# Performance work log

Hardware: AMD Instinct MI355X
Metric: run time of the kernel (lower is better)

## Reference

```python
import jax, jax.numpy as jnp
import numpy as np
from jax import lax

B = 512
P_KEEP = 0.5  # base dropout keep probability (p=0.5)


def conv(x, w, b, pad):
    y = lax.conv_general_dilated(x, w, (1, 1), [(pad, pad), (pad, pad)],
                                 dimension_numbers=('NCHW', 'OIHW', 'NCHW'))
    return y + b[None, :, None, None]


def maxpool3s2(x):
    return lax.reduce_window(x, -jnp.inf, lax.max, (1, 1, 3, 3), (1, 1, 2, 2), 'VALID')


def eb_linear(p_out, a, W):
    # Excitation backprop through a linear layer (bias ignored).
    # p_out: [B, out] marginal winning probs at layer output
    # a:     [B, in]  (non-negative) activations at layer input
    # W:     [out, in]
    Wp = jnp.maximum(W, 0.0)
    z = a @ Wp.T                              # [B, out]
    s = jnp.where(z > 0, p_out / z, 0.0)      # [B, out]
    return a * (s @ Wp)                       # [B, in]


def setup_inputs() -> dict:
    key = jax.random.key(0)
    ks = jax.random.split(key, 16)

    def w(k, shape, fan_in):
        return (jax.random.normal(k, shape, jnp.float32) / np.sqrt(fan_in)).astype(jnp.float32)

    return {
        'x': jax.random.normal(ks[0], (B, 3, 32, 32), jnp.float32),
        'noise': jax.random.uniform(ks[1], (B, 2048), jnp.float32),
        'conv1_w': w(ks[2], (96, 3, 5, 5), 3 * 25),
        'conv1_b': jnp.zeros((96,), jnp.float32),
        'conv2_w': w(ks[3], (128, 96, 5, 5), 96 * 25),
        'conv2_b': jnp.zeros((128,), jnp.float32),
        'conv3_w': w(ks[4], (256, 128, 5, 5), 128 * 25),
        'conv3_b': jnp.zeros((256,), jnp.float32),
        'fc1_w': w(ks[5], (2048, 1024), 1024),
        'fc1_b': jnp.zeros((2048,), jnp.float32),
        'fc2_w': w(ks[6], (2048, 2048), 2048),
        'fc2_b': jnp.zeros((2048,), jnp.float32),
        'fc3_w': w(ks[7], (10, 2048), 2048),
        'fc3_b': jnp.zeros((10,), jnp.float32),
        'label': jax.random.randint(ks[8], (B,), 0, 10),
    }


def reference(x, noise, conv1_w, conv1_b, conv2_w, conv2_b, conv3_w, conv3_b,
              fc1_w, fc1_b, fc2_w, fc2_b, fc3_w, fc3_b, label):
    h1 = maxpool3s2(jax.nn.relu(conv(x, conv1_w, conv1_b, 1)))   # [B,96,14,14]
    h2 = maxpool3s2(jax.nn.relu(conv(h1, conv2_w, conv2_b, 2)))  # [B,128,6,6]
    h3 = maxpool3s2(jax.nn.relu(conv(h2, conv3_w, conv3_b, 2)))  # [B,256,2,2]
    h4 = h3.reshape(h3.shape[0], -1)                             # [B,1024]
    h5 = jax.nn.relu(h4 @ fc1_w.T + fc1_b)                       # [B,2048]

    # --- Excitation backprop through latterModel (fc2 -> relu -> fc3), batched ---
    h6_eb = jax.nn.relu(h5 @ fc2_w.T + fc2_b)                    # [B,2048]
    p_out = jax.nn.one_hot(label, 10, dtype=h5.dtype)            # [B,10]
    p_h6 = eb_linear(p_out, h6_eb, fc3_w)                        # [B,2048]
    pebs = eb_linear(p_h6, h5, fc2_w)                            # [B,2048]

    # --- Excitation Dropout mask ---
    N = pebs.shape[1]
    num = (1.0 - P_KEEP) * (N - 1) * pebs
    retain_p = 1.0 - num / (num + P_KEEP * (1.0 - pebs))         # [B,2048]
    mask = (noise < retain_p).astype(h5.dtype)
    h_ed = jnp.where(retain_p > 0, h5 * mask / retain_p, 0.0)

    h6 = jax.nn.relu(h_ed @ fc2_w.T + fc2_b)                     # [B,2048]
    return h6 @ fc3_w.T + fc3_b                                  # [B,10]
```

## Files before the change

kernel.cpp:

```cpp
#include <hip/hip_runtime.h>
#include <hip/hip_bf16.h>


typedef __attribute__((ext_vector_type(8))) short bf16x8;
typedef __attribute__((ext_vector_type(4))) float f32x4;

__device__ __forceinline__ void split_bf16(float x, ushort& h, ushort& l) {
    __hip_bfloat16 bh = __float2bfloat16(x);
    float fh = __bfloat162float(bh);
    __hip_bfloat16 bl = __float2bfloat16(x - fh);
    h = *(ushort*)&bh;
    l = *(ushort*)&bl;
}

__device__ __forceinline__ void split3_bf16(float x, ushort& a, ushort& b,
                                            ushort& c) {
    __hip_bfloat16 ba = __float2bfloat16(x);
    float fa = __bfloat162float(ba);
    float r = x - fa;
    __hip_bfloat16 bb = __float2bfloat16(r);
    float fb = __bfloat162float(bb);
    __hip_bfloat16 bc = __float2bfloat16(r - fb);
    a = *(ushort*)&ba;
    b = *(ushort*)&bb;
    c = *(ushort*)&bc;
}

__device__ __forceinline__ void gld_lds16(const void* g, void* l) {
    __builtin_amdgcn_global_load_lds(
        (const __attribute__((address_space(1))) unsigned int*)g,
        (__attribute__((address_space(3))) unsigned int*)l, 16, 0, 0);
}

__global__ void zero_k(float4* __restrict__ p, int n4) {
    int idx = blockIdx.x * 256 + threadIdx.x;
    int stride = gridDim.x * 256;
    float4 z = {0.f, 0.f, 0.f, 0.f};
    for (int i = idx; i < n4; i += stride) p[i] = z;
}

__global__ void transw_k(const float* __restrict__ in, float* __restrict__ out,
                         int OC, int K) {
    int idx = blockIdx.x * 256 + threadIdx.x;
    if (idx >= OC * K) return;
    int oc = idx / K, k = idx % K;
    out[k * OC + oc] = in[idx];
}

__global__ void splitw_k(const float* __restrict__ in, ushort* __restrict__ hi,
                         ushort* __restrict__ lo, int OC, int IC) {
    int idx = blockIdx.x * 256 + threadIdx.x;
    if (idx >= OC * IC * 25) return;
    int oc = idx / (IC * 25);
    int r = idx % (IC * 25);
    int ic = r / 25, tap = r % 25;
    float v = in[idx];
    ushort h, l;
    split_bf16(v, h, l);
    size_t k = (size_t)oc * IC * 25 + tap * IC + ic;
    hi[k] = h;
    lo[k] = l;
}

__global__ void splitw3_k(const float* __restrict__ in, ushort* __restrict__ out,
                          int off, int total) {
    int idx = blockIdx.x * 256 + threadIdx.x;
    if (idx >= total) return;
    ushort a, b, c;
    split3_bf16(in[idx], a, b, c);
    out[idx] = a;
    out[idx + off] = b;
    out[idx + 2 * off] = c;
}

__global__ __launch_bounds__(256) void splitw3t_relu_k(
        const float* __restrict__ in, ushort* __restrict__ out, int off) {
    __shared__ float tile[64][65];
    const int bx = blockIdx.x & 31, by = blockIdx.x >> 5;
    const int j = threadIdx.x & 63, i0 = threadIdx.x >> 6;
    for (int i = i0; i < 64; i += 4)
        tile[i][j] = in[(size_t)(by * 64 + i) * 2048 + bx * 64 + j];
    __syncthreads();
    for (int r = i0; r < 64; r += 4) {
        float x = fmaxf(tile[j][r], 0.f);
        ushort a, b, c;
        split3_bf16(x, a, b, c);
        size_t o = (size_t)(bx * 64 + r) * 2048 + by * 64 + j;
        out[o] = a;
        out[o + off] = b;
        out[o + 2 * off] = c;
    }
}

__global__ __launch_bounds__(256) void conv1_v3(
        const float* __restrict__ x, const float* __restrict__ w1t,
        const float* __restrict__ b1, ushort* __restrict__ h1hi,
        ushort* __restrict__ h1lo) {
    __shared__ float simg[3 * 34 * 34];
    __shared__ float c1s[8][904];
    const int b = blockIdx.x, oc0 = blockIdx.y * 8, t = threadIdx.x;

    for (int i = t; i < 3 * 34 * 34; i += 256) simg[i] = 0.f;
    __syncthreads();
    for (int i = t; i < 3072; i += 256) {
        int ic = i >> 10, r = (i >> 5) & 31, c = i & 31;
        simg[ic * 1156 + (r + 1) * 34 + (c + 1)] = x[(size_t)b * 3072 + i];
    }
    __syncthreads();

    int base[4];
    bool valid[4];
#pragma unroll
    for (int j = 0; j < 4; j++) {
        int p = t + j * 256;
        valid[j] = p < 900;
        int oh = p / 30, ow = p % 30;
        base[j] = valid[j] ? oh * 34 + ow : 0;
    }

    float acc[4][8];
#pragma unroll
    for (int j = 0; j < 4; j++)
#pragma unroll
        for (int u = 0; u < 8; u++) acc[j][u] = 0.f;

#pragma unroll 1
    for (int ic = 0; ic < 3; ic++) {
        const int icb = ic * 1156;
#pragma unroll 1
        for (int kh = 0; kh < 5; kh++) {
#pragma unroll
            for (int kw = 0; kw < 5; kw++) {
                const float4* wr =
                    (const float4*)&w1t[(ic * 25 + kh * 5 + kw) * 96 + oc0];
                float4 w0 = wr[0], w1v = wr[1];
#pragma unroll
                for (int j = 0; j < 4; j++) {
                    float v = simg[icb + base[j] + kh * 34 + kw];
#pragma unroll
                    for (int u = 0; u < 4; u++) {
                        acc[j][u] = fmaf((&w0.x)[u], v, acc[j][u]);
                        acc[j][u + 4] = fmaf((&w1v.x)[u], v, acc[j][u + 4]);
                    }
                }
            }
        }
    }
#pragma unroll
    for (int j = 0; j < 4; j++)
        if (valid[j]) {
            int p = t + j * 256;
#pragma unroll
            for (int u = 0; u < 8; u++) c1s[u][p] = acc[j][u];
        }
    __syncthreads();
    if (t < 196) {
        const int ph = t / 14, pw = t % 14;
        ushort hv[8], lv[8];
#pragma unroll
        for (int u = 0; u < 8; u++) {
            float m = c1s[u][(2 * ph) * 30 + 2 * pw];
#pragma unroll
            for (int q = 1; q < 9; q++) {
                int dy = q / 3, dx = q % 3;
                m = fmaxf(m, c1s[u][(2 * ph + dy) * 30 + 2 * pw + dx]);
            }
            float o = fmaxf(m + b1[oc0 + u], 0.f);
            split_bf16(o, hv[u], lv[u]);
        }
        size_t ob = (((size_t)b * 18 + ph + 2) * 18 + pw + 2) * 96 + oc0;
        *(bf16x8*)&h1hi[ob] = *(bf16x8*)&hv[0];
        *(bf16x8*)&h1lo[ob] = *(bf16x8*)&lv[0];
    }
}

template <int BM, int IC, int H, int W, int OH, int OW, int OC, int NM>
__global__ __launch_bounds__(256, 2) void convmfma5_k(
        const ushort* __restrict__ ah, int aoff,
        const ushort* __restrict__ wh, int boff,
        const float* __restrict__ bias, float* __restrict__ C) {
    constexpr int K = 25 * IC;
    constexpr int MI = BM / 32;
    constexpr int G = NM * (OC / 128);
    __shared__ ushort At[2][BM * 64];
    __shared__ ushort Bt[2][128 * 64];
    const int t = threadIdx.x;
    const int lane = t & 63, wv = t >> 6;
    const int id = blockIdx.x;
    const int id2 = (id & 7) * (G >> 3) + (id >> 3);
    const int n0 = (id2 / NM) * 128;
    const int m0 = (id2 % NM) * BM;
    const int wm = (wv >> 1) * (BM / 2);
    const int wn = (wv & 1) * 64;

    const int srow = lane >> 3;
    const int slot = lane & 7;
    const int part = slot ^ srow;
    const bool hiA = part < 4;
    const int pk = (part & 3) * 8;

    int arb[MI];
#pragma unroll
    for (int rr = 0; rr < MI; rr++) {
        int r = wv * (BM / 4) + rr * 8 + srow;
        int m = m0 + r;
        int b = m / (OH * OW), pxy = m % (OH * OW);
        int oh = pxy / OW, ow = pxy % OW;
        arb[rr] = ((b * H + oh) * W + ow) * IC + pk;
    }
    const ushort* __restrict__ aptr = ah + (hiA ? 0 : aoff);
    size_t brb[4];
#pragma unroll
    for (int rr = 0; rr < 4; rr++) {
        int r = wv * 32 + rr * 8 + srow;
        brb[rr] = (size_t)(n0 + r) * K + pk;
    }
    const ushort* __restrict__ bptr = wh + (hiA ? 0 : boff);

    f32x4 acc[MI][4];
#pragma unroll
    for (int i = 0; i < MI; i++)
#pragma unroll
        for (int j = 0; j < 4; j++) acc[i][j] = (f32x4)(0.f);

    const int q = lane >> 4;
    const int fr = lane & 15;

    auto stage = [&](int buf, int k0s) {
        const int tap = k0s / IC;
        const int koff = ((tap / 5) * W + (tap % 5)) * IC + (k0s - tap * IC);
#pragma unroll
        for (int rr = 0; rr < MI; rr++)
            gld_lds16(aptr + arb[rr] + koff,
                      &At[buf][(wv * (BM / 4) + rr * 8) * 64]);
#pragma unroll
        for (int rr = 0; rr < 4; rr++)
            gld_lds16(bptr + brb[rr] + k0s,
                      &Bt[buf][(wv * 32 + rr * 8) * 64]);
    };

    stage(0, 0);
    __syncthreads();

    int cur = 0;
#pragma unroll 1
    for (int k0 = 0; k0 < K; k0 += 32) {
        bf16x8 afh[MI], afl[MI], bfh[4], bfl[4];
#pragma unroll
        for (int i = 0; i < MI; i++) {
            int row = wm + fr + i * 16;
            afh[i] = *(const bf16x8*)&At[cur][row * 64 + ((q ^ (row & 7)) << 3)];
            afl[i] = *(const bf16x8*)&At[cur][row * 64 + (((4 | q) ^ (row & 7)) << 3)];
        }
#pragma unroll
        for (int j = 0; j < 4; j++) {
            int row = wn + fr + j * 16;
            bfh[j] = *(const bf16x8*)&Bt[cur][row * 64 + ((q ^ (row & 7)) << 3)];
            bfl[j] = *(const bf16x8*)&Bt[cur][row * 64 + (((4 | q) ^ (row & 7)) << 3)];
        }
        const int nxt = k0 + 32;
        if (nxt < K) stage(cur ^ 1, nxt);

#pragma unroll
        for (int i = 0; i < MI; i++)
#pragma unroll
            for (int j = 0; j < 4; j++) {
                acc[i][j] = __builtin_amdgcn_mfma_f32_16x16x32_bf16(
                    afh[i], bfh[j], acc[i][j], 0, 0, 0);
                acc[i][j] = __builtin_amdgcn_mfma_f32_16x16x32_bf16(
                    afh[i], bfl[j], acc[i][j], 0, 0, 0);
                acc[i][j] = __builtin_amdgcn_mfma_f32_16x16x32_bf16(
                    afl[i], bfh[j], acc[i][j], 0, 0, 0);
            }
        __syncthreads();
        cur ^= 1;
    }

    const int crow0 = (lane >> 4) * 4;
    const int ccol = lane & 15;
#pragma unroll
    for (int i = 0; i < MI; i++) {
        int gm = m0 + wm + i * 16 + crow0;
#pragma unroll
        for (int j = 0; j < 4; j++) {
            int gn = n0 + wn + j * 16 + ccol;
            float bb = bias[gn];
#pragma unroll
            for (int r = 0; r < 4; r++)
                C[(size_t)(gm + r) * OC + gn] = acc[i][j][r] + bb;
        }
    }
}

__global__ void pool2_k(const float* __restrict__ in, ushort* __restrict__ ohi,
                        ushort* __restrict__ olo) {
    int idx = blockIdx.x * 256 + threadIdx.x;
    if (idx >= 512 * 36 * 128) return;
    int c = idx & 127;
    int tmp = idx >> 7;
    int pw = tmp % 6;
    int tmp2 = tmp / 6;
    int ph = tmp2 % 6;
    int b = tmp2 / 6;
    size_t base = (((size_t)b * 14 + 2 * ph) * 14 + 2 * pw) * 128 + c;
    float m = -3.4e38f;
#pragma unroll
    for (int dy = 0; dy < 3; dy++)
#pragma unroll
        for (int dx = 0; dx < 3; dx++)
            m = fmaxf(m, in[base + (dy * 14 + dx) * 128]);
    float v = fmaxf(m, 0.f);
    ushort h, l;
    split_bf16(v, h, l);
    size_t o = (((size_t)b * 10 + ph + 2) * 10 + pw + 2) * 128 + c;
    ohi[o] = h;
    olo[o] = l;
}

__global__ void pool3_k(const float* __restrict__ in, float* __restrict__ h3) {
    int idx = blockIdx.x * 256 + threadIdx.x;
    if (idx >= 512 * 4 * 256) return;
    int c = idx & 255;
    int pw = (idx >> 8) & 1;
    int ph = (idx >> 9) & 1;
    int b = idx >> 10;
    size_t base = (((size_t)b * 6 + 2 * ph) * 6 + 2 * pw) * 256 + c;
    float m = -3.4e38f;
#pragma unroll
    for (int dy = 0; dy < 3; dy++)
#pragma unroll
        for (int dx = 0; dx < 3; dx++)
            m = fmaxf(m, in[base + (dy * 6 + dx) * 256]);
    h3[(size_t)b * 1024 + c * 4 + ph * 2 + pw] = fmaxf(m, 0.f);
}

template <int TRANSB, int RELUW, int BIAS, int RELUOUT, int DUAL>
__global__ __launch_bounds__(256, 2) void gemm2_k(
        const float* __restrict__ A, const float* __restrict__ Bm,
        const float* __restrict__ bias, float* __restrict__ C,
        float* __restrict__ C2, int K, int N) {
    __shared__ float As[16][36];
    __shared__ float Bs[16][68];
    __shared__ float Bs2[DUAL ? 16 : 1][68];
    const int t = threadIdx.x;
    const int n0 = blockIdx.x * 64;
    const int m0 = blockIdx.y * 32;
    const int tm = t >> 5, tn = t & 31;

    float acc[8];
    float acc2[DUAL ? 8 : 1];
#pragma unroll
    for (int i = 0; i < 8; i++) acc[i] = 0.f;
    if constexpr (DUAL) {
#pragma unroll
        for (int i = 0; i < 8; i++) acc2[i] = 0.f;
    }

    const int r4 = t >> 2, k4 = (t & 3) << 2;

    for (int k0 = 0; k0 < K; k0 += 16) {
        float4 av;
        if (t < 128) av = *(const float4*)&A[(size_t)(m0 + r4) * K + k0 + k4];
        float4 bv;
        if constexpr (TRANSB) {
            bv = *(const float4*)&Bm[(size_t)(n0 + r4) * K + k0 + k4];
        } else {
            bv = *(const float4*)&Bm[(size_t)(k0 + (t >> 4)) * N + n0 + ((t & 15) << 2)];
        }
        if constexpr (RELUW) {
            bv.x = fmaxf(bv.x, 0.f); bv.y = fmaxf(bv.y, 0.f);
            bv.z = fmaxf(bv.z, 0.f); bv.w = fmaxf(bv.w, 0.f);
        }
        __syncthreads();
        if (t < 128) {
            As[k4 + 0][r4] = av.x; As[k4 + 1][r4] = av.y;
            As[k4 + 2][r4] = av.z; As[k4 + 3][r4] = av.w;
        }
        if constexpr (TRANSB) {
            Bs[k4 + 0][r4] = bv.x; Bs[k4 + 1][r4] = bv.y;
            Bs[k4 + 2][r4] = bv.z; Bs[k4 + 3][r4] = bv.w;
            if constexpr (DUAL) {
                Bs2[k4 + 0][r4] = fmaxf(bv.x, 0.f);
                Bs2[k4 + 1][r4] = fmaxf(bv.y, 0.f);
                Bs2[k4 + 2][r4] = fmaxf(bv.z, 0.f);
                Bs2[k4 + 3][r4] = fmaxf(bv.w, 0.f);
            }
        } else {
            *(float4*)&Bs[t >> 4][(t & 15) << 2] = bv;
        }
        __syncthreads();
#pragma unroll
        for (int kk = 0; kk < 16; kk++) {
            float4 a4 = *(const float4*)&As[kk][tm * 4];
            float2 b2 = *(const float2*)&Bs[kk][tn * 2];
            const float* ap = &a4.x;
            const float* bp = &b2.x;
            if constexpr (DUAL) {
                float2 b2p = *(const float2*)&Bs2[kk][tn * 2];
                const float* bpp = &b2p.x;
#pragma unroll
                for (int i = 0; i < 4; i++)
#pragma unroll
                    for (int j = 0; j < 2; j++) {
                        acc[i * 2 + j] = fmaf(ap[i], bp[j], acc[i * 2 + j]);
                        acc2[i * 2 + j] = fmaf(ap[i], bpp[j], acc2[i * 2 + j]);
                    }
            } else {
#pragma unroll
                for (int i = 0; i < 4; i++)
#pragma unroll
                    for (int j = 0; j < 2; j++)
                        acc[i * 2 + j] = fmaf(ap[i], bp[j], acc[i * 2 + j]);
            }
        }
    }

#pragma unroll
    for (int i = 0; i < 4; i++) {
        size_t row = (size_t)(m0 + tm * 4 + i) * N + n0 + tn * 2;
        float2 o;
#pragma unroll
        for (int j = 0; j < 2; j++) {
            float v = acc[i * 2 + j];
            if constexpr (BIAS) v += bias[n0 + tn * 2 + j];
            if constexpr (RELUOUT) v = fmaxf(v, 0.f);
            (&o.x)[j] = v;
        }
        *(float2*)&C[row] = o;
        if constexpr (DUAL) {
            float2 o2;
#pragma unroll
            for (int j = 0; j < 2; j++) (&o2.x)[j] = acc2[i * 2 + j];
            *(float2*)&C2[row] = o2;
        }
    }
}

template <int BIAS, int RELUOUT, int DUAL>
__global__ __launch_bounds__(256, 2) void gemmfc_k(
        const float* __restrict__ A, const ushort* __restrict__ B3, int boff,
        const float* __restrict__ bias, float* __restrict__ C,
        float* __restrict__ C2, int K, int N) {
    __shared__ ushort Aa[32][40], Ab[32][40], Ac[32][40];
    __shared__ ushort Ba[64][40], Bb[64][40], Bc[64][40];
    const int t = threadIdx.x;
    const int n0 = blockIdx.x * 64;
    const int m0 = blockIdx.y * 32;
    const int lane = t & 63, wv = t >> 6;
    const int wm = (wv >> 1) * 16, wn = (wv & 1) * 32;
    const int fr = lane & 15, kp = (lane >> 4) * 8;

    f32x4 acc[2], acc2[DUAL ? 2 : 1];
#pragma unroll
    for (int j = 0; j < 2; j++) acc[j] = (f32x4)(0.f);
    if constexpr (DUAL) {
#pragma unroll
        for (int j = 0; j < 2; j++) acc2[j] = (f32x4)(0.f);
    }

    const int ar = t >> 2, ak = (t & 3) * 8;

    for (int k0 = 0; k0 < K; k0 += 32) {
        float4 a0, a1;
        if (t < 128) {
            a0 = *(const float4*)&A[(size_t)(m0 + ar) * K + k0 + ak];
            a1 = *(const float4*)&A[(size_t)(m0 + ar) * K + k0 + ak + 4];
        }
        size_t bidx = (size_t)(n0 + ar) * K + k0 + ak;
        bf16x8 b0 = *(const bf16x8*)&B3[bidx];
        bf16x8 b1 = *(const bf16x8*)&B3[bidx + boff];
        bf16x8 b2 = *(const bf16x8*)&B3[bidx + 2 * (size_t)boff];
        __syncthreads();
        if (t < 128) {
            ushort sa[8], sb[8], sc[8];
#pragma unroll
            for (int e = 0; e < 4; e++)
                split3_bf16((&a0.x)[e], sa[e], sb[e], sc[e]);
#pragma unroll
            for (int e = 0; e < 4; e++)
                split3_bf16((&a1.x)[e], sa[4 + e], sb[4 + e], sc[4 + e]);
            *(bf16x8*)&Aa[ar][ak] = *(bf16x8*)sa;
            *(bf16x8*)&Ab[ar][ak] = *(bf16x8*)sb;
            *(bf16x8*)&Ac[ar][ak] = *(bf16x8*)sc;
        }
        *(bf16x8*)&Ba[ar][ak] = b0;
        *(bf16x8*)&Bb[ar][ak] = b1;
        *(bf16x8*)&Bc[ar][ak] = b2;
        __syncthreads();

        bf16x8 fa = *(const bf16x8*)&Aa[wm + fr][kp];
        bf16x8 fb = *(const bf16x8*)&Ab[wm + fr][kp];
        bf16x8 fc = *(const bf16x8*)&Ac[wm + fr][kp];
#pragma unroll
        for (int j = 0; j < 2; j++) {
            int row = wn + j * 16 + fr;
            bf16x8 ga = *(const bf16x8*)&Ba[row][kp];
            bf16x8 gb = *(const bf16x8*)&Bb[row][kp];
            bf16x8 gc = *(const bf16x8*)&Bc[row][kp];
            acc[j] = __builtin_amdgcn_mfma_f32_16x16x32_bf16(fa, ga, acc[j], 0, 0, 0);
            acc[j] = __builtin_amdgcn_mfma_f32_16x16x32_bf16(fa, gb, acc[j], 0, 0, 0);
            acc[j] = __builtin_amdgcn_mfma_f32_16x16x32_bf16(fb, ga, acc[j], 0, 0, 0);
            acc[j] = __builtin_amdgcn_mfma_f32_16x16x32_bf16(fa, gc, acc[j], 0, 0, 0);
            acc[j] = __builtin_amdgcn_mfma_f32_16x16x32_bf16(fc, ga, acc[j], 0, 0, 0);
            acc[j] = __builtin_amdgcn_mfma_f32_16x16x32_bf16(fb, gb, acc[j], 0, 0, 0);
            if constexpr (DUAL) {
                bf16x8 msk = ga >> 15;
                bf16x8 ra = ga & ~msk;
                bf16x8 rb = gb & ~msk;
                bf16x8 rc = gc & ~msk;
                acc2[j] = __builtin_amdgcn_mfma_f32_16x16x32_bf16(fa, ra, acc2[j], 0, 0, 0);
                acc2[j] = __builtin_amdgcn_mfma_f32_16x16x32_bf16(fa, rb, acc2[j], 0, 0, 0);
                acc2[j] = __builtin_amdgcn_mfma_f32_16x16x32_bf16(fb, ra, acc2[j], 0, 0, 0);
                acc2[j] = __builtin_amdgcn_mfma_f32_16x16x32_bf16(fa, rc, acc2[j], 0, 0, 0);
                acc2[j] = __builtin_amdgcn_mfma_f32_16x16x32_bf16(fc, ra, acc2[j], 0, 0, 0);
                acc2[j] = __builtin_amdgcn_mfma_f32_16x16x32_bf16(fb, rb, acc2[j], 0, 0, 0);
            }
        }
    }

    const int gm0 = m0 + wm + (lane >> 4) * 4;
#pragma unroll
    for (int j = 0; j < 2; j++) {
        int gn = n0 + wn + j * 16 + fr;
        float bb = BIAS ? bias[gn] : 0.f;
#pragma unroll
        for (int r = 0; r < 4; r++) {
            float v = acc[j][r] + bb;
            if constexpr (RELUOUT) v = fmaxf(v, 0.f);
            C[(size_t)(gm0 + r) * N + gn] = v;
            if constexpr (DUAL) C2[(size_t)(gm0 + r) * N + gn] = acc2[j][r];
        }
    }
}

__global__ __launch_bounds__(256) void zlab_k(
        const float* __restrict__ h6eb, const float* __restrict__ w3,
        const int* __restrict__ label, float* __restrict__ zlab) {
    __shared__ float red[4];
    const int b = blockIdx.x, t = threadIdx.x;
    const int lab = label[b];
    const float4* hp = (const float4*)(h6eb + (size_t)b * 2048);
    const float4* wp = (const float4*)(w3 + (size_t)lab * 2048);
    float s = 0.f;
    for (int i = t; i < 512; i += 256) {
        float4 h = hp[i], w = wp[i];
        s += h.x * fmaxf(w.x, 0.f) + h.y * fmaxf(w.y, 0.f) +
             h.z * fmaxf(w.z, 0.f) + h.w * fmaxf(w.w, 0.f);
    }
#pragma unroll
    for (int off = 32; off > 0; off >>= 1) s += __shfl_down(s, off, 64);
    if ((t & 63) == 0) red[t >> 6] = s;
    __syncthreads();
    if (t == 0) zlab[b] = red[0] + red[1] + red[2] + red[3];
}

__global__ void s2_k(const float* __restrict__ h6eb, const float* __restrict__ z2,
                     const float* __restrict__ w3, const int* __restrict__ label,
                     const float* __restrict__ zlab, float* __restrict__ s2) {
    int idx = blockIdx.x * 256 + threadIdx.x;
    int b = idx >> 11, j = idx & 2047;
    float zl = zlab[b], zv = z2[idx];
    float v = 0.f;
    if (zl > 0.f && zv > 0.f) {
        float wp = fmaxf(w3[(size_t)label[b] * 2048 + j], 0.f);
        v = h6eb[idx] * wp / (zl * zv);
    }
    s2[idx] = v;
}

__global__ void edrop_k(const float* __restrict__ h5, const float* __restrict__ t,
                        const float* __restrict__ noise, float* __restrict__ hed) {
    int idx = blockIdx.x * 256 + threadIdx.x;
    float pe = h5[idx] * t[idx];
    float num = 1023.5f * pe;
    float retain = 1.f - num / (num + 0.5f * (1.f - pe));
    float m = (noise[idx] < retain) ? 1.f : 0.f;
    hed[idx] = (retain > 0.f) ? h5[idx] * m / retain : 0.f;
}

__global__ void fc3_out_k(const float* __restrict__ h6, const float* __restrict__ w,
                          const float* __restrict__ bias, float* __restrict__ out) {
    int idx = blockIdx.x * 256 + threadIdx.x;
    if (idx >= 5120) return;
    int b = idx / 10, c = idx % 10;
    const float4* hp = (const float4*)(h6 + (size_t)b * 2048);
    const float4* wp = (const float4*)(w + (size_t)c * 2048);
    float s = 0.f;
    for (int i = 0; i < 512; i++) {
        float4 h = hp[i], ww = wp[i];
        s += h.x * ww.x + h.y * ww.y + h.z * ww.z + h.w * ww.w;
    }
    out[idx] = s + bias[c];
}

extern "C" void kernel_launch(void* const* d_in, const int* in_sizes, int n_in,
                              void* d_out, int out_size, void* d_ws, size_t ws_size,
                              hipStream_t stream) {
    const float* x       = (const float*)d_in[0];
    const float* noise   = (const float*)d_in[1];
    const float* conv1_w = (const float*)d_in[2];
    const float* conv1_b = (const float*)d_in[3];
    const float* conv2_w = (const float*)d_in[4];
    const float* conv2_b = (const float*)d_in[5];
    const float* conv3_w = (const float*)d_in[6];
    const float* conv3_b = (const float*)d_in[7];
    const float* fc1_w   = (const float*)d_in[8];
    const float* fc1_b   = (const float*)d_in[9];
    const float* fc2_w   = (const float*)d_in[10];
    const float* fc2_b   = (const float*)d_in[11];
    const float* fc3_w   = (const float*)d_in[12];
    const float* fc3_b   = (const float*)d_in[13];
    const int*   label   = (const int*)d_in[14];
    float* out = (float*)d_out;

    const size_t N_H1 = (size_t)512 * 18 * 18 * 96;
    const size_t N_C2 = (size_t)512 * 14 * 14 * 128;
    const size_t N_H2 = (size_t)512 * 10 * 10 * 128;
    const size_t N_H3 = (size_t)512 * 1024;

    float* ws = (float*)d_ws;
    ushort* h1hi = (ushort*)ws;
    ushort* h1lo = h1hi + N_H1;
    float* c3 = ws;
    float* c2 = ws + N_H1;
    float* h5   = c2;
    float* h6eb = c2 + 1 * 1048576;
    float* z2   = c2 + 2 * 1048576;
    float* s2   = c2 + 3 * 1048576;
    float* tb   = c2 + 4 * 1048576;
    float* hed  = c2 + 5 * 1048576;
    float* h6   = c2 + 6 * 1048576;
    float* zlab = c2 + 7 * 1048576;
    ushort* h2hi = (ushort*)(ws + N_H1 + N_C2);
    ushort* h2lo = h2hi + N_H2;
    float* h3  = ws + N_H1 + N_C2 + N_H2;
    float* w1t = h3 + N_H3;
    ushort* w2sh = (ushort*)(w1t + 7200);
    ushort* w2sl = w2sh + 307200;
    ushort* w3sh = w2sl + 307200;
    ushort* w3sl = w3sh + 819200;
    ushort* w23  = w3sl + 819200;
    ushort* w2rt = w23 + 3 * 4194304;

    transw_k<<<(75 * 96 + 255) / 256, 256, 0, stream>>>(conv1_w, w1t, 96, 75);
    splitw_k<<<(307200 + 255) / 256, 256, 0, stream>>>(conv2_w, w2sh, w2sl, 128, 96);
    splitw_k<<<(819200 + 255) / 256, 256, 0, stream>>>(conv3_w, w3sh, w3sl, 256, 128);
    splitw3_k<<<16384, 256, 0, stream>>>(fc2_w, w23, 4194304, 4194304);
    splitw3t_relu_k<<<1024, 256, 0, stream>>>(fc2_w, w2rt, 4194304);

    zero_k<<<2048, 256, 0, stream>>>((float4*)h1hi, (int)(N_H1 / 4));
    zero_k<<<2048, 256, 0, stream>>>((float4*)h2hi, (int)(N_H2 / 4));

    conv1_v3<<<dim3(512, 12), 256, 0, stream>>>(x, w1t, conv1_b, h1hi, h1lo);
    convmfma5_k<128, 96, 18, 18, 14, 14, 128, 784><<<784, 256, 0, stream>>>(
        h1hi, (int)N_H1, w2sh, 307200, conv2_b, c2);
    pool2_k<<<(512 * 36 * 128 + 255) / 256, 256, 0, stream>>>(c2, h2hi, h2lo);
    convmfma5_k<64, 128, 10, 10, 6, 6, 256, 288><<<576, 256, 0, stream>>>(
        h2hi, (int)N_H2, w3sh, 819200, conv3_b, c3);
    pool3_k<<<(512 * 4 * 256 + 255) / 256, 256, 0, stream>>>(c3, h3);

    gemm2_k<1, 0, 1, 1, 0><<<dim3(32, 16), 256, 0, stream>>>(
        h3, fc1_w, fc1_b, h5, nullptr, 1024, 2048);

    gemmfc_k<1, 1, 1><<<dim3(32, 16), 256, 0, stream>>>(
        h5, w23, 4194304, fc2_b, h6eb, z2, 2048, 2048);

    zlab_k<<<512, 256, 0, stream>>>(h6eb, fc3_w, label, zlab);
    s2_k<<<4096, 256, 0, stream>>>(h6eb, z2, fc3_w, label, zlab, s2);

    gemmfc_k<0, 0, 0><<<dim3(32, 16), 256, 0, stream>>>(
        s2, w2rt, 4194304, nullptr, tb, nullptr, 2048, 2048);

    edrop_k<<<4096, 256, 0, stream>>>(h5, tb, noise, hed);

    gemmfc_k<1, 1, 0><<<dim3(32, 16), 256, 0, stream>>>(
        hed, w23, 4194304, fc2_b, h6, nullptr, 2048, 2048);

    fc3_out_k<<<20, 256, 0, stream>>>(h6, fc3_w, fc3_b, out);
}
```

Before: 839.0 us.

## Stage conv weights through registers and run fc1 on split-bf16 MFMA GEMM

The conv MFMA kernel now keeps a single LDS buffer for the weight tile. Weights are prefetched into registers one step ahead and written to LDS at the start of each iteration, and the kernel adds explicit waitcnt/barrier handling, setprio around the MFMA block, and a higher occupancy hint. Separately, fc1 moves from a scalar fp32 SIMT GEMM to the existing three-way bf16-split MFMA gemmfc kernel, which needs an extra weight-split pass. The changes aim to cut LDS pressure, raise occupancy, and speed up fc1, but they add register pressure and an extra preprocessing kernel.

New measurement: 855.3 us. No clear change (+1.9%).

```diff
diff --git a/kernel.cpp b/kernel.cpp
--- a/kernel.cpp
+++ b/kernel.cpp
@@ -175,7 +175,7 @@
 }
 
 template <int BM, int IC, int H, int W, int OH, int OW, int OC, int NM>
-__global__ __launch_bounds__(256, 2) void convmfma5_k(
+__global__ __launch_bounds__(256, 3) void convmfma6_k(
         const ushort* __restrict__ ah, int aoff,
         const ushort* __restrict__ wh, int boff,
         const float* __restrict__ bias, float* __restrict__ C) {
@@ -183,7 +183,7 @@
     constexpr int MI = BM / 32;
     constexpr int G = NM * (OC / 128);
     __shared__ ushort At[2][BM * 64];
-    __shared__ ushort Bt[2][128 * 64];
+    __shared__ ushort Bt[128 * 64];
     const int t = threadIdx.x;
     const int lane = t & 63, wv = t >> 6;
     const int id = blockIdx.x;
@@ -226,25 +226,33 @@
     const int q = lane >> 4;
     const int fr = lane & 15;
 
-    auto stage = [&](int buf, int k0s) {
+    auto stageA = [&](int buf, int k0s) {
         const int tap = k0s / IC;
         const int koff = ((tap / 5) * W + (tap % 5)) * IC + (k0s - tap * IC);
 #pragma unroll
         for (int rr = 0; rr < MI; rr++)
             gld_lds16(aptr + arb[rr] + koff,
                       &At[buf][(wv * (BM / 4) + rr * 8) * 64]);
-#pragma unroll
-        for (int rr = 0; rr < 4; rr++)
-            gld_lds16(bptr + brb[rr] + k0s,
-                      &Bt[buf][(wv * 32 + rr * 8) * 64]);
     };
 
-    stage(0, 0);
-    __syncthreads();
+    bf16x8 bregs[4];
+#pragma unroll
+    for (int rr = 0; rr < 4; rr++)
+        bregs[rr] = *(const bf16x8*)&bptr[brb[rr]];
+    stageA(0, 0);
+    asm volatile("s_waitcnt vmcnt(0)" ::: "memory");
+    __builtin_amdgcn_s_barrier();
 
     int cur = 0;
 #pragma unroll 1
     for (int k0 = 0; k0 < K; k0 += 32) {
+#pragma unroll
+        for (int rr = 0; rr < 4; rr++)
+            *(bf16x8*)&Bt[(wv * 32 + rr * 8 + srow) * 64 + slot * 8] = bregs[rr];
+        const int nxt = k0 + 32;
+        if (nxt < K) stageA(cur ^ 1, nxt);
+        asm volatile("s_waitcnt lgkmcnt(0)" ::: "memory");
+        __builtin_amdgcn_s_barrier();
         bf16x8 afh[MI], afl[MI], bfh[4], bfl[4];
 #pragma unroll
         for (int i = 0; i < MI; i++) {
@@ -255,12 +263,15 @@
 #pragma unroll
         for (int j = 0; j < 4; j++) {
             int row = wn + fr + j * 16;
-            bfh[j] = *(const bf16x8*)&Bt[cur][row * 64 + ((q ^ (row & 7)) << 3)];
-            bfl[j] = *(const bf16x8*)&Bt[cur][row * 64 + (((4 | q) ^ (row & 7)) << 3)];
-        }
-        const int nxt = k0 + 32;
-        if (nxt < K) stage(cur ^ 1, nxt);
-
+            bfh[j] = *(const bf16x8*)&Bt[row * 64 + ((q ^ (row & 7)) << 3)];
+            bfl[j] = *(const bf16x8*)&Bt[row * 64 + (((4 | q) ^ (row & 7)) << 3)];
+        }
+        if (nxt < K) {
+#pragma unroll
+            for (int rr = 0; rr < 4; rr++)
+                bregs[rr] = *(const bf16x8*)&bptr[brb[rr] + nxt];
+        }
+        __builtin_amdgcn_s_setprio(1);
 #pragma unroll
         for (int i = 0; i < MI; i++)
 #pragma unroll
@@ -272,7 +283,9 @@
                 acc[i][j] = __builtin_amdgcn_mfma_f32_16x16x32_bf16(
                     afl[i], bfh[j], acc[i][j], 0, 0, 0);
             }
-        __syncthreads();
+        __builtin_amdgcn_s_setprio(0);
+        asm volatile("s_waitcnt vmcnt(0)" ::: "memory");
+        __builtin_amdgcn_s_barrier();
         cur ^= 1;
     }
 
@@ -332,108 +345,6 @@
         for (int dx = 0; dx < 3; dx++)
             m = fmaxf(m, in[base + (dy * 6 + dx) * 256]);
     h3[(size_t)b * 1024 + c * 4 + ph * 2 + pw] = fmaxf(m, 0.f);
-}
-
-template <int TRANSB, int RELUW, int BIAS, int RELUOUT, int DUAL>
-__global__ __launch_bounds__(256, 2) void gemm2_k(
-        const float* __restrict__ A, const float* __restrict__ Bm,
-        const float* __restrict__ bias, float* __restrict__ C,
-        float* __restrict__ C2, int K, int N) {
-    __shared__ float As[16][36];
-    __shared__ float Bs[16][68];
-    __shared__ float Bs2[DUAL ? 16 : 1][68];
-    const int t = threadIdx.x;
-    const int n0 = blockIdx.x * 64;
-    const int m0 = blockIdx.y * 32;
-    const int tm = t >> 5, tn = t & 31;
-
-    float acc[8];
-    float acc2[DUAL ? 8 : 1];
-#pragma unroll
-    for (int i = 0; i < 8; i++) acc[i] = 0.f;
-    if constexpr (DUAL) {
-#pragma unroll
-        for (int i = 0; i < 8; i++) acc2[i] = 0.f;
-    }
-
-    const int r4 = t >> 2, k4 = (t & 3) << 2;
-
-    for (int k0 = 0; k0 < K; k0 += 16) {
-        float4 av;
-        if (t < 128) av = *(const float4*)&A[(size_t)(m0 + r4) * K + k0 + k4];
-        float4 bv;
-        if constexpr (TRANSB) {
-            bv = *(const float4*)&Bm[(size_t)(n0 + r4) * K + k0 + k4];
-        } else {
-            bv = *(const float4*)&Bm[(size_t)(k0 + (t >> 4)) * N + n0 + ((t & 15) << 2)];
-        }
-        if constexpr (RELUW) {
-            bv.x = fmaxf(bv.x, 0.f); bv.y = fmaxf(bv.y, 0.f);
-            bv.z = fmaxf(bv.z, 0.f); bv.w = fmaxf(bv.w, 0.f);
-        }
-        __syncthreads();
-        if (t < 128) {
-            As[k4 + 0][r4] = av.x; As[k4 + 1][r4] = av.y;
-            As[k4 + 2][r4] = av.z; As[k4 + 3][r4] = av.w;
-        }
-        if constexpr (TRANSB) {
-            Bs[k4 + 0][r4] = bv.x; Bs[k4 + 1][r4] = bv.y;
-            Bs[k4 + 2][r4] = bv.z; Bs[k4 + 3][r4] = bv.w;
-            if constexpr (DUAL) {
-                Bs2[k4 + 0][r4] = fmaxf(bv.x, 0.f);
-                Bs2[k4 + 1][r4] = fmaxf(bv.y, 0.f);
-                Bs2[k4 + 2][r4] = fmaxf(bv.z, 0.f);
-                Bs2[k4 + 3][r4] = fmaxf(bv.w, 0.f);
-            }
-        } else {
-            *(float4*)&Bs[t >> 4][(t & 15) << 2] = bv;
-        }
-        __syncthreads();
-#pragma unroll
-        for (int kk = 0; kk < 16; kk++) {
-            float4 a4 = *(const float4*)&As[kk][tm * 4];
-            float2 b2 = *(const float2*)&Bs[kk][tn * 2];
-            const float* ap = &a4.x;
-            const float* bp = &b2.x;
-            if constexpr (DUAL) {
-                float2 b2p = *(const float2*)&Bs2[kk][tn * 2];
-                const float* bpp = &b2p.x;
-#pragma unroll
-                for (int i = 0; i < 4; i++)
-#pragma unroll
-                    for (int j = 0; j < 2; j++) {
-                        acc[i * 2 + j] = fmaf(ap[i], bp[j], acc[i * 2 + j]);
-                        acc2[i * 2 + j] = fmaf(ap[i], bpp[j], acc2[i * 2 + j]);
-                    }
-            } else {
-#pragma unroll
-                for (int i = 0; i < 4; i++)
-#pragma unroll
-                    for (int j = 0; j < 2; j++)
-                        acc[i * 2 + j] = fmaf(ap[i], bp[j], acc[i * 2 + j]);
-            }
-        }
-    }
-
-#pragma unroll
-    for (int i = 0; i < 4; i++) {
-        size_t row = (size_t)(m0 + tm * 4 + i) * N + n0 + tn * 2;
-        float2 o;
-#pragma unroll
-        for (int j = 0; j < 2; j++) {
-            float v = acc[i * 2 + j];
-            if constexpr (BIAS) v += bias[n0 + tn * 2 + j];
-            if constexpr (RELUOUT) v = fmaxf(v, 0.f);
-            (&o.x)[j] = v;
-        }
-        *(float2*)&C[row] = o;
-        if constexpr (DUAL) {
-            float2 o2;
-#pragma unroll
-            for (int j = 0; j < 2; j++) (&o2.x)[j] = acc2[i * 2 + j];
-            *(float2*)&C2[row] = o2;
-        }
-    }
 }
 
 template <int BIAS, int RELUOUT, int DUAL>
@@ -641,26 +552,28 @@
     ushort* w3sl = w3sh + 819200;
     ushort* w23  = w3sl + 819200;
     ushort* w2rt = w23 + 3 * 4194304;
+    ushort* w13  = w2rt + 3 * 4194304;
 
     transw_k<<<(75 * 96 + 255) / 256, 256, 0, stream>>>(conv1_w, w1t, 96, 75);
     splitw_k<<<(307200 + 255) / 256, 256, 0, stream>>>(conv2_w, w2sh, w2sl, 128, 96);
     splitw_k<<<(819200 + 255) / 256, 256, 0, stream>>>(conv3_w, w3sh, w3sl, 256, 128);
     splitw3_k<<<16384, 256, 0, stream>>>(fc2_w, w23, 4194304, 4194304);
     splitw3t_relu_k<<<1024, 256, 0, stream>>>(fc2_w, w2rt, 4194304);
+    splitw3_k<<<8192, 256, 0, stream>>>(fc1_w, w13, 2097152, 2097152);
 
     zero_k<<<2048, 256, 0, stream>>>((float4*)h1hi, (int)(N_H1 / 4));
     zero_k<<<2048, 256, 0, stream>>>((float4*)h2hi, (int)(N_H2 / 4));
 
     conv1_v3<<<dim3(512, 12), 256, 0, stream>>>(x, w1t, conv1_b, h1hi, h1lo);
-    convmfma5_k<128, 96, 18, 18, 14, 14, 128, 784><<<784, 256, 0, stream>>>(
+    convmfma6_k<128, 96, 18, 18, 14, 14, 128, 784><<<784, 256, 0, stream>>>(
         h1hi, (int)N_H1, w2sh, 307200, conv2_b, c2);
     pool2_k<<<(512 * 36 * 128 + 255) / 256, 256, 0, stream>>>(c2, h2hi, h2lo);
-    convmfma5_k<64, 128, 10, 10, 6, 6, 256, 288><<<576, 256, 0, stream>>>(
+    convmfma6_k<64, 128, 10, 10, 6, 6, 256, 288><<<576, 256, 0, stream>>>(
         h2hi, (int)N_H2, w3sh, 819200, conv3_b, c3);
     pool3_k<<<(512 * 4 * 256 + 255) / 256, 256, 0, stream>>>(c3, h3);
 
-    gemm2_k<1, 0, 1, 1, 0><<<dim3(32, 16), 256, 0, stream>>>(
-        h3, fc1_w, fc1_b, h5, nullptr, 1024, 2048);
+    gemmfc_k<1, 1, 0><<<dim3(32, 16), 256, 0, stream>>>(
+        h3, w13, 2097152, fc1_b, h5, nullptr, 1024, 2048);
 
     gemmfc_k<1, 1, 1><<<dim3(32, 16), 256, 0, stream>>>(
         h5, w23, 4194304, fc2_b, h6eb, z2, 2048, 2048);
```
